# Kernel optimization log

Measured on AMD Instinct MI355X. Metric: run time of the kernel, lower is better.

The kernel has to match this reference:

```python
import jax, jax.numpy as jnp
import numpy as np

SEQ_LEN = 16384
D = 2048
K = 50          # tagset size
START = 48
STOP = 49
NEG = -10000.0


def setup_inputs() -> dict:
    key = jax.random.key(0)
    k1, k2, k3, k4 = jax.random.split(key, 4)
    input_var = jax.random.normal(k1, (SEQ_LEN, D), jnp.float32)
    tags = jax.random.randint(k2, (SEQ_LEN,), 0, 48, dtype=jnp.int32)  # real tags only
    W = jax.random.normal(k3, (K, D), jnp.float32) * 0.02              # hidden2tag weight
    b = jnp.zeros((K,), jnp.float32)                                   # hidden2tag bias
    transitions = jax.random.normal(k4, (K, K), jnp.float32) * 0.1
    # match the torch init: no transition into START, none out of STOP
    transitions = transitions.at[START, :].set(NEG).at[:, STOP].set(NEG)
    return {"input_var": input_var, "tags": tags, "W": W, "b": b, "transitions": transitions}


def reference(input_var, tags, W, b, transitions):
    # dropout in eval mode == identity (faithful deterministic forward)
    feats = input_var @ W.T + b  # [T, K] emission scores

    # --- CRF forward algorithm (log partition) ---
    alpha0 = jnp.full((K,), NEG, jnp.float32).at[START].set(0.0)

    def step(alpha, feat):
        # tag_var[i, j] = alpha[j] + transitions[i, j] + feat[i]
        s = alpha[None, :] + transitions           # [K, K]
        m = jnp.max(s, axis=1)                     # stable log-sum-exp
        alpha_new = feat + m + jnp.log(jnp.sum(jnp.exp(s - m[:, None]), axis=1))
        return alpha_new, None

    alpha, _ = jax.lax.scan(step, alpha0, feats)
    term = alpha + transitions[STOP]
    mt = jnp.max(term)
    forward_score = mt + jnp.log(jnp.sum(jnp.exp(term - mt)))

    # --- gold path score ---
    pad_start = jnp.concatenate([jnp.array([START], dtype=tags.dtype), tags])
    pad_stop = jnp.concatenate([tags, jnp.array([STOP], dtype=tags.dtype)])
    gold = (jnp.sum(transitions[pad_stop, pad_start])
            + jnp.sum(feats[jnp.arange(SEQ_LEN), tags]))

    return forward_score - gold
```

## Files before the change

kernel.cpp:

```cpp
#include <hip/hip_runtime.h>

typedef unsigned short u16;
typedef unsigned int u32;
typedef __bf16 b16x8 __attribute__((ext_vector_type(8)));
typedef float f32x16 __attribute__((ext_vector_type(16)));

#define SEQ   16384
#define DM    2048
#define KT    50
#define NST   48
#define NSP   49

__device__ __forceinline__ int perm64(int g){
  int q = (g>>2)&3;
  return (q==1 || q==2) ? (g^12) : g;
}
__device__ __forceinline__ u16 bfb(float f){
  __bf16 b = (__bf16)f;
  return __builtin_bit_cast(u16, b);
}
__device__ __forceinline__ int pk2(float a, float b){
  return (int)((u32)bfb(a) | ((u32)bfb(b) << 16));
}
__device__ __forceinline__ b16x8 cast8(int4 v){ return __builtin_bit_cast(b16x8, v); }

__device__ __forceinline__ f32x16 mfma_(b16x8 a, b16x8 b, f32x16 c){
  return __builtin_amdgcn_mfma_f32_32x32x16_bf16(a, b, c, 0, 0, 0);
}

__device__ __forceinline__ void mm64(const b16x8 A[2][4], const b16x8 B[4][2], f32x16 acc[2][2]){
#pragma unroll
  for (int mi=0; mi<2; ++mi)
#pragma unroll
    for (int ni=0; ni<2; ++ni){
      f32x16 a;
#pragma unroll
      for (int q=0;q<16;q++) a[q] = 0.0f;
#pragma unroll
      for (int kt=0; kt<4; ++kt) a = mfma_(A[mi][kt], B[kt][ni], a);
      acc[mi][ni] = a;
    }
}

__device__ __forceinline__ void repack(const f32x16 acc[2][2], b16x8 B[4][2]){
#pragma unroll
  for (int kb=0; kb<4; ++kb){
    const int mi = kb>>1, t = kb&1;
#pragma unroll
    for (int ni=0; ni<2; ++ni){
      int4 dw;
      dw.x = pk2(acc[mi][ni][8*t+0], acc[mi][ni][8*t+1]);
      dw.y = pk2(acc[mi][ni][8*t+2], acc[mi][ni][8*t+3]);
      dw.z = pk2(acc[mi][ni][8*t+4], acc[mi][ni][8*t+5]);
      dw.w = pk2(acc[mi][ni][8*t+6], acc[mi][ni][8*t+7]);
      B[kb][ni] = cast8(dw);
    }
  }
}

template<int PERM>
__device__ __forceinline__ void ident_frags(b16x8 B[4][2], int lane){
  const int h = lane>>5, j0 = lane&31;
#pragma unroll
  for (int kt=0; kt<4; ++kt)
#pragma unroll
    for (int ni=0; ni<2; ++ni){
      const int col = j0 + 32*ni;
      int d[4];
#pragma unroll
      for (int dd=0; dd<4; ++dd){
        int r0 = 16*kt + 8*h + 2*dd, r1 = r0 + 1;
        int p0 = PERM ? perm64(r0) : r0;
        int p1 = PERM ? perm64(r1) : r1;
        d[dd] = (int)((p0==col ? 0x3F80u : 0u) | ((p1==col ? 0x3F80u : 0u) << 16));
      }
      int4 v; v.x=d[0]; v.y=d[1]; v.z=d[2]; v.w=d[3];
      B[kt][ni] = cast8(v);
    }
}

__device__ __forceinline__ float acc_wave_max(const f32x16 acc[2][2]){
  float m = 0.0f;
#pragma unroll
  for (int mi=0;mi<2;mi++)
#pragma unroll
    for (int ni=0;ni<2;ni++)
#pragma unroll
      for (int q=0;q<16;q++) m = fmaxf(m, acc[mi][ni][q]);
#pragma unroll
  for (int o=32;o>=1;o>>=1) m = fmaxf(m, __shfl_xor(m, o, 64));
  return m;
}

template<int PROW>
__device__ __forceinline__ void store_mat_lds(u16* mat, const f32x16 acc[2][2], float inv, int lane){
  const int h = lane>>5, j0 = lane&31;
#pragma unroll
  for (int mi=0;mi<2;mi++)
#pragma unroll
    for (int ni=0;ni<2;ni++)
#pragma unroll
      for (int r=0;r<16;r++){
        int gp = 32*mi + (r&3) + 8*(r>>2) + 4*h;
        int a = PROW ? perm64(gp) : gp;
        int b = perm64(32*ni + j0);
        mat[a*64 + (b ^ ((a&7)<<3))] = bfb(acc[mi][ni][r]*inv);
      }
}
template<int PROW>
__device__ __forceinline__ void store_mat_glob(u16* mat, const f32x16 acc[2][2], float inv, int lane){
  const int h = lane>>5, j0 = lane&31;
#pragma unroll
  for (int mi=0;mi<2;mi++)
#pragma unroll
    for (int ni=0;ni<2;ni++)
#pragma unroll
      for (int r=0;r<16;r++){
        int gp = 32*mi + (r&3) + 8*(r>>2) + 4*h;
        int a = PROW ? perm64(gp) : gp;
        int b = perm64(32*ni + j0);
        mat[a*64 + b] = bfb(acc[mi][ni][r]*inv);
      }
}
__device__ __forceinline__ void load_afrag_lds(const u16* mat, b16x8 A[2][4], int lane){
  const int h = lane>>5, i0 = lane&31;
#pragma unroll
  for (int mi=0;mi<2;mi++)
#pragma unroll
    for (int kt=0;kt<4;kt++){
      int i = 32*mi + i0;
      int cb = (16*kt + 8*h) ^ ((i&7)<<3);
      A[mi][kt] = cast8(*(const int4*)(mat + i*64 + cb));
    }
}
__device__ __forceinline__ void load_afrag_glob(const u16* mat, b16x8 A[2][4], int lane){
  const int h = lane>>5, i0 = lane&31;
#pragma unroll
  for (int mi=0;mi<2;mi++)
#pragma unroll
    for (int kt=0;kt<4;kt++){
      int i = 32*mi + i0;
      A[mi][kt] = cast8(*(const int4*)(mat + i*64 + 16*kt + 8*h));
    }
}

__global__ void k_prep(const float* __restrict__ W, const float* __restrict__ T,
                       u16* __restrict__ Wp, u16* __restrict__ E){
  int tid = blockIdx.x*256 + threadIdx.x;
  int n = gridDim.x*256;
  for (int idx = tid; idx < 64*DM; idx += n){
    int r = idx >> 11, d = idx & 2047;
    Wp[idx] = (r < KT) ? bfb(W[r*DM + d]) : (u16)0;
  }
  for (int idx = tid; idx < 64*64; idx += n){
    int a = idx >> 6, b = idx & 63;
    int pa = perm64(a);
    E[idx] = (pa < KT && b < KT) ? bfb(__expf(T[pa*50 + b])) : (u16)0;
  }
}

__global__ __launch_bounds__(256, 2) void k_gemm(const float* __restrict__ in,
      const u16* __restrict__ Wp, const float* __restrict__ bias,
      const int* __restrict__ tags, float* __restrict__ feats, float* __restrict__ gout){
  const int w = threadIdx.x>>6, lane = threadIdx.x&63;
  const int h = lane>>5, i0 = lane&31;
  const int blk = blockIdx.x;
  const int row = blk*32 + i0;
  f32x16 acc0, acc1;
#pragma unroll
  for (int q=0;q<16;q++){ acc0[q]=0.f; acc1[q]=0.f; }
  const float* pa  = in + (size_t)row*DM + w*512 + 8*h;
  const u16*   pb0 = Wp + (size_t)i0*DM + w*512 + 8*h;
  const u16*   pb1 = Wp + (size_t)(i0+32)*DM + w*512 + 8*h;
#pragma unroll 4
  for (int s=0;s<32;s++){
    float4 fa = *(const float4*)(pa + s*16);
    float4 fb = *(const float4*)(pa + s*16 + 4);
    b16x8 av;
    av[0]=(__bf16)fa.x; av[1]=(__bf16)fa.y; av[2]=(__bf16)fa.z; av[3]=(__bf16)fa.w;
    av[4]=(__bf16)fb.x; av[5]=(__bf16)fb.y; av[6]=(__bf16)fb.z; av[7]=(__bf16)fb.w;
    b16x8 b0 = cast8(*(const int4*)(pb0 + s*16));
    b16x8 b1 = cast8(*(const int4*)(pb1 + s*16));
    acc0 = mfma_(av, b0, acc0);
    acc1 = mfma_(av, b1, acc1);
  }
  __shared__ float planes[4][32][64];
#pragma unroll
  for (int r=0;r<16;r++){
    int g = (r&3) + 8*(r>>2) + 4*h;
    planes[w][g][i0]    = acc0[r];
    planes[w][g][i0+32] = acc1[r];
  }
  __syncthreads();
  __shared__ float tile[32][66];
  for (int cidx = threadIdx.x; cidx < 2048; cidx += 256){
    int g = cidx>>6, c = cidx&63;
    float v = planes[0][g][c]+planes[1][g][c]+planes[2][g][c]+planes[3][g][c];
    tile[g][c] = (c<KT) ? (v + bias[c]) : -1e4f;
  }
  __syncthreads();
  __shared__ float mrow[32];
  if (threadIdx.x < 32){
    int g = threadIdx.x;
    float mx = -1e30f;
    for (int c=0;c<KT;c++) mx = fmaxf(mx, tile[g][c]);
    mrow[g] = mx;
    int t = blk*32 + g;
    gout[t] = tile[g][tags[t]] - mx;
  }
  __syncthreads();
  for (int cidx = threadIdx.x; cidx < 2048; cidx += 256){
    int g = cidx>>6, c = cidx&63;
    feats[(size_t)(blk*32+g)*64 + c] = (c<KT) ? (tile[g][c] - mrow[g]) : -1e4f;
  }
}

__global__ __launch_bounds__(512, 2) void k_scan(const float* __restrict__ feats,
        const u16* __restrict__ Emat, u16* __restrict__ M1, float* __restrict__ S1){
  const int w = threadIdx.x >> 6, lane = threadIdx.x & 63;
  const int h = lane>>5;
  const int blk = blockIdx.x;
  const int t0 = (blk*8 + w)*8;
  __shared__ __align__(16) float u_lds[8][64];
  __shared__ __align__(16) u16 mats[8][4096];
  __shared__ float logs[8];

  b16x8 Af[2][4];
  load_afrag_glob(Emat, Af, lane);
  b16x8 Bf[4][2];
  ident_frags<0>(Bf, lane);
  const int pl = perm64(lane);
  float x = feats[(size_t)t0*64 + pl];
  f32x16 acc[2][2];
#pragma unroll
  for (int s=0;s<8;s++){
    u_lds[w][lane] = __expf(x);
    if (s<7) x = feats[(size_t)(t0+s+1)*64 + pl];
    mm64(Af, Bf, acc);
    float uu0[16], uu1[16];
#pragma unroll
    for (int k2=0;k2<4;k2++){
      float4 v0 = *(const float4*)&u_lds[w][      8*k2 + 4*h];
      float4 v1 = *(const float4*)&u_lds[w][32 +  8*k2 + 4*h];
      uu0[4*k2+0]=v0.x; uu0[4*k2+1]=v0.y; uu0[4*k2+2]=v0.z; uu0[4*k2+3]=v0.w;
      uu1[4*k2+0]=v1.x; uu1[4*k2+1]=v1.y; uu1[4*k2+2]=v1.z; uu1[4*k2+3]=v1.w;
    }
#pragma unroll
    for (int ni=0;ni<2;ni++)
#pragma unroll
      for (int r=0;r<16;r++){
        acc[0][ni][r] *= uu0[r];
        acc[1][ni][r] *= uu1[r];
      }
    repack(acc, Bf);
  }
  float m = acc_wave_max(acc);
  float inv = 1.0f/m;
  store_mat_lds<1>(mats[w], acc, inv, lane);
  if (lane==0) logs[w] = __logf(m);
  __syncthreads();
  if (w==0){
    float slog = logs[0]+logs[1]+logs[2]+logs[3]+logs[4]+logs[5]+logs[6]+logs[7];
    b16x8 Bc[4][2]; ident_frags<1>(Bc, lane);
    f32x16 a2[2][2];
#pragma unroll 1
    for (int m8=0;m8<8;m8++){
      b16x8 Am[2][4];
      load_afrag_lds(mats[m8], Am, lane);
      mm64(Am, Bc, a2);
      repack(a2, Bc);
    }
    float m2 = acc_wave_max(a2);
    slog += __logf(m2);
    store_mat_glob<0>(M1 + (size_t)blk*4096, a2, 1.0f/m2, lane);
    if (lane==0) S1[blk] = slog;
  }
}

__global__ __launch_bounds__(64) void k_comb8(const u16* __restrict__ Min, const float* __restrict__ Sin,
      u16* __restrict__ Mout, float* __restrict__ Sout){
  const int lane = threadIdx.x & 63;
  const int blk = blockIdx.x;
  b16x8 Bc[4][2]; ident_frags<1>(Bc, lane);
  f32x16 a2[2][2];
  float slog = 0.f;
#pragma unroll 1
  for (int m=0;m<8;m++){
    b16x8 Am[2][4];
    load_afrag_glob(Min + (size_t)(blk*8+m)*4096, Am, lane);
    slog += Sin[blk*8+m];
    mm64(Am, Bc, a2);
    repack(a2, Bc);
  }
  float mx = acc_wave_max(a2);
  slog += __logf(mx);
  store_mat_glob<0>(Mout + (size_t)blk*4096, a2, 1.0f/mx, lane);
  if (lane==0) Sout[blk] = slog;
}

__global__ __launch_bounds__(512, 2) void k_final(const u16* __restrict__ M2, const float* __restrict__ S2,
      const float* __restrict__ T, const int* __restrict__ tags,
      const float* __restrict__ gvec, float* __restrict__ out){
  const int w = threadIdx.x>>6, lane = threadIdx.x&63;
  __shared__ __align__(16) u16 mats[8][4096];
  __shared__ float logs[8];
  __shared__ float alpha[64];
  __shared__ float red[512];
  __shared__ float slog_sh;
  {
    b16x8 Bc[4][2]; ident_frags<1>(Bc, lane);
    f32x16 a2[2][2];
    float sl = 0.f;
#pragma unroll 1
    for (int m=0;m<4;m++){
      b16x8 Am[2][4];
      load_afrag_glob(M2 + (size_t)(w*4+m)*4096, Am, lane);
      sl += S2[w*4+m];
      mm64(Am, Bc, a2);
      repack(a2, Bc);
    }
    float mx = acc_wave_max(a2);
    sl += __logf(mx);
    store_mat_lds<0>(mats[w], a2, 1.0f/mx, lane);
    if (lane==0) logs[w] = sl;
  }
  __syncthreads();
  if (w==0){
    b16x8 Bc[4][2]; ident_frags<1>(Bc, lane);
    f32x16 a2[2][2];
#pragma unroll 1
    for (int m=0;m<8;m++){
      b16x8 Am[2][4];
      load_afrag_lds(mats[m], Am, lane);
      mm64(Am, Bc, a2);
      repack(a2, Bc);
    }
    float sl = logs[0]+logs[1]+logs[2]+logs[3]+logs[4]+logs[5]+logs[6]+logs[7];
    if ((lane&31)==16){
      const int h = lane>>5;
#pragma unroll
      for (int mi=0;mi<2;mi++)
#pragma unroll
        for (int r=0;r<16;r++){
          int gp = 32*mi + (r&3) + 8*(r>>2) + 4*h;
          alpha[gp] = a2[mi][1][r];
        }
    }
    if (lane==0) slog_sh = sl;
  }
  float part = 0.f;
  for (int t = threadIdx.x; t < SEQ; t += 512) part += gvec[t];
  for (int idx = threadIdx.x; idx < SEQ+1; idx += 512){
    int s0 = (idx==0) ? NST : tags[idx-1];
    int s1 = (idx<SEQ) ? tags[idx] : NSP;
    part += T[s1*50 + s0];
  }
  red[threadIdx.x] = part;
  for (int st=256; st>0; st>>=1){
    __syncthreads();
    if (threadIdx.x < st) red[threadIdx.x] += red[threadIdx.x + st];
  }
  __syncthreads();
  if (threadIdx.x < 64){
    float a = alpha[lane];
    float term = (lane < KT && a > 0.f) ? (__logf(a) + slog_sh + T[NSP*50 + lane]) : -1e30f;
    float tm = term;
#pragma unroll
    for (int o=32;o>=1;o>>=1) tm = fmaxf(tm, __shfl_xor(tm, o, 64));
    float e = __expf(term - tm);
#pragma unroll
    for (int o=32;o>=1;o>>=1) e += __shfl_xor(e, o, 64);
    if (threadIdx.x == 0) out[0] = (tm + __logf(e)) - red[0];
  }
}

extern "C" void kernel_launch(void* const* d_in, const int* in_sizes, int n_in,
                              void* d_out, int out_size, void* d_ws, size_t ws_size,
                              hipStream_t stream) {
  (void)in_sizes; (void)n_in; (void)out_size; (void)ws_size;
  const float* input = (const float*)d_in[0];
  const int*   tags  = (const int*)  d_in[1];
  const float* W     = (const float*)d_in[2];
  const float* bias  = (const float*)d_in[3];
  const float* T     = (const float*)d_in[4];

  char* ws = (char*)d_ws;
  float* feats = (float*)(ws + 0);
  float* gvec  = (float*)(ws + 4194304);
  u16*   Wp    = (u16*)  (ws + 4259840);
  u16*   Emat  = (u16*)  (ws + 4521984);
  u16*   M1    = (u16*)  (ws + 4530176);
  float* S1    = (float*)(ws + 6627328);
  u16*   M2    = (u16*)  (ws + 6628352);
  float* S2    = (float*)(ws + 6890496);

  k_prep <<<256, 256, 0, stream>>>(W, T, Wp, Emat);
  k_gemm <<<512, 256, 0, stream>>>(input, Wp, bias, tags, feats, gvec);
  k_scan <<<256, 512, 0, stream>>>(feats, Emat, M1, S1);
  k_comb8<<<32,  64,  0, stream>>>(M1, S1, M2, S2);
  k_final<<<1,   512, 0, stream>>>(M2, S2, T, tags, gvec, (float*)d_out);
}
```

Measured before the change: 111.0 us.

## Fuse CRF pipeline into two kernels with LDS-tiled GEMM and last-block reduction

Collapses five launches into two. The prep kernel is removed: W is converted to bf16 inside a new double-buffered, LDS-swizzled GEMM with 64-row tiles, and exp(T) is built in LDS per scan block. The gold-path score is folded into the GEMM as per-block partials. The scan does 16 steps per wave with half the blocks, and the comb8 and final stages run inside the last-arriving scan block via an atomic counter. This cuts launch overhead and intermediate global traffic, but it serialises the final reduction on one block and relies on an atomic counter that is reset by GEMM block 0.

```diff
diff --git a/kernel.cpp b/kernel.cpp
--- a/kernel.cpp
+++ b/kernel.cpp
@@ -53,6 +53,21 @@
       dw.y = pk2(acc[mi][ni][8*t+2], acc[mi][ni][8*t+3]);
       dw.z = pk2(acc[mi][ni][8*t+4], acc[mi][ni][8*t+5]);
       dw.w = pk2(acc[mi][ni][8*t+6], acc[mi][ni][8*t+7]);
+      B[kb][ni] = cast8(dw);
+    }
+  }
+}
+__device__ __forceinline__ void repack_s(const f32x16 acc[2][2], b16x8 B[4][2], float s){
+#pragma unroll
+  for (int kb=0; kb<4; ++kb){
+    const int mi = kb>>1, t = kb&1;
+#pragma unroll
+    for (int ni=0; ni<2; ++ni){
+      int4 dw;
+      dw.x = pk2(acc[mi][ni][8*t+0]*s, acc[mi][ni][8*t+1]*s);
+      dw.y = pk2(acc[mi][ni][8*t+2]*s, acc[mi][ni][8*t+3]*s);
+      dw.z = pk2(acc[mi][ni][8*t+4]*s, acc[mi][ni][8*t+5]*s);
+      dw.w = pk2(acc[mi][ni][8*t+6]*s, acc[mi][ni][8*t+7]*s);
       B[kb][ni] = cast8(dw);
     }
   }
@@ -144,98 +159,147 @@
     }
 }
 
-__global__ void k_prep(const float* __restrict__ W, const float* __restrict__ T,
-                       u16* __restrict__ Wp, u16* __restrict__ E){
-  int tid = blockIdx.x*256 + threadIdx.x;
-  int n = gridDim.x*256;
-  for (int idx = tid; idx < 64*DM; idx += n){
-    int r = idx >> 11, d = idx & 2047;
-    Wp[idx] = (r < KT) ? bfb(W[r*DM + d]) : (u16)0;
-  }
-  for (int idx = tid; idx < 64*64; idx += n){
-    int a = idx >> 6, b = idx & 63;
-    int pa = perm64(a);
-    E[idx] = (pa < KT && b < KT) ? bfb(__expf(T[pa*50 + b])) : (u16)0;
-  }
-}
-
-__global__ __launch_bounds__(256, 2) void k_gemm(const float* __restrict__ in,
-      const u16* __restrict__ Wp, const float* __restrict__ bias,
-      const int* __restrict__ tags, float* __restrict__ feats, float* __restrict__ gout){
-  const int w = threadIdx.x>>6, lane = threadIdx.x&63;
-  const int h = lane>>5, i0 = lane&31;
-  const int blk = blockIdx.x;
-  const int row = blk*32 + i0;
-  f32x16 acc0, acc1;
-#pragma unroll
-  for (int q=0;q<16;q++){ acc0[q]=0.f; acc1[q]=0.f; }
-  const float* pa  = in + (size_t)row*DM + w*512 + 8*h;
-  const u16*   pb0 = Wp + (size_t)i0*DM + w*512 + 8*h;
-  const u16*   pb1 = Wp + (size_t)(i0+32)*DM + w*512 + 8*h;
-#pragma unroll 4
-  for (int s=0;s<32;s++){
-    float4 fa = *(const float4*)(pa + s*16);
-    float4 fb = *(const float4*)(pa + s*16 + 4);
-    b16x8 av;
-    av[0]=(__bf16)fa.x; av[1]=(__bf16)fa.y; av[2]=(__bf16)fa.z; av[3]=(__bf16)fa.w;
-    av[4]=(__bf16)fb.x; av[5]=(__bf16)fb.y; av[6]=(__bf16)fb.z; av[7]=(__bf16)fb.w;
-    b16x8 b0 = cast8(*(const int4*)(pb0 + s*16));
-    b16x8 b1 = cast8(*(const int4*)(pb1 + s*16));
-    acc0 = mfma_(av, b0, acc0);
-    acc1 = mfma_(av, b1, acc1);
-  }
-  __shared__ float planes[4][32][64];
+__global__ __launch_bounds__(512, 2) void k_gemm(const float* __restrict__ in,
+      const int* __restrict__ tags, const float* __restrict__ W,
+      const float* __restrict__ bias, const float* __restrict__ T,
+      float* __restrict__ feats, float* __restrict__ gpart, int* __restrict__ counter){
+  __shared__ __align__(16) char smem[65536];
+  u16* const bA = (u16*)smem;
+  u16* const bB = (u16*)(smem + 32768);
+  const int t = threadIdx.x;
+  const int w = t>>6, lane = t&63;
+  const int j0 = lane&31, h = lane>>5;
+  const int rh = w&1, ch = (w>>1)&1, kq = (w>>2)&1;
+  const int row0 = blockIdx.x*64;
+  const int aswz = (j0&7)<<3;
+  if (blockIdx.x==0 && t==0) *counter = 0;
+
+  float rA[2][8], rB[2][8];
+  f32x16 acc;
+#pragma unroll
+  for (int q=0;q<16;q++) acc[q]=0.f;
+
+#define LOADCHUNK(kc)                                                       \
+  { _Pragma("unroll")                                                       \
+    for (int i=0;i<2;i++){                                                  \
+      int g=(i<<9)+t; int r=g>>4, c8=g&15;                                  \
+      const float* p = in + (size_t)(row0+r)*DM + (kc)*128 + c8*8;          \
+      float4 f0=*(const float4*)p, f1=*(const float4*)(p+4);                \
+      rA[i][0]=f0.x; rA[i][1]=f0.y; rA[i][2]=f0.z; rA[i][3]=f0.w;           \
+      rA[i][4]=f1.x; rA[i][5]=f1.y; rA[i][6]=f1.z; rA[i][7]=f1.w;           \
+      if (r < KT){                                                          \
+        const float* q2 = W + (size_t)r*DM + (kc)*128 + c8*8;               \
+        float4 g0=*(const float4*)q2, g1=*(const float4*)(q2+4);            \
+        rB[i][0]=g0.x; rB[i][1]=g0.y; rB[i][2]=g0.z; rB[i][3]=g0.w;         \
+        rB[i][4]=g1.x; rB[i][5]=g1.y; rB[i][6]=g1.z; rB[i][7]=g1.w;         \
+      } else {                                                              \
+        _Pragma("unroll") for (int z=0;z<8;z++) rB[i][z]=0.f;               \
+      }                                                                     \
+    } }
+#define WRITECHUNK(d)                                                       \
+  { _Pragma("unroll")                                                       \
+    for (int i=0;i<2;i++){                                                  \
+      int g=(i<<9)+t; int r=g>>4, c8=g&15;                                  \
+      int off = r*128 + ((c8*8) ^ ((r&7)<<3));                              \
+      int4 da; da.x=pk2(rA[i][0],rA[i][1]); da.y=pk2(rA[i][2],rA[i][3]);    \
+      da.z=pk2(rA[i][4],rA[i][5]); da.w=pk2(rA[i][6],rA[i][7]);             \
+      *(int4*)(bA + (d)*8192 + off) = da;                                   \
+      int4 db; db.x=pk2(rB[i][0],rB[i][1]); db.y=pk2(rB[i][2],rB[i][3]);    \
+      db.z=pk2(rB[i][4],rB[i][5]); db.w=pk2(rB[i][6],rB[i][7]);             \
+      *(int4*)(bB + (d)*8192 + off) = db;                                   \
+    } }
+
+  LOADCHUNK(0); WRITECHUNK(0);
+  __syncthreads();
+  for (int kc=0; kc<16; ++kc){
+    const int d = kc & 1;
+    if (kc < 15) LOADCHUNK(kc+1);
+    const u16* Arow = bA + d*8192 + (32*rh + j0)*128;
+    const u16* Brow = bB + d*8192 + (32*ch + j0)*128;
+#pragma unroll
+    for (int kk=0;kk<4;kk++){
+      const int kt = kq*4 + kk;
+      b16x8 aF = cast8(*(const int4*)(Arow + ((kt*16 + h*8) ^ aswz)));
+      b16x8 bF = cast8(*(const int4*)(Brow + ((kt*16 + h*8) ^ aswz)));
+      acc = mfma_(aF, bF, acc);
+    }
+    if (kc < 15) WRITECHUNK(d^1);
+    __syncthreads();
+  }
+#undef LOADCHUNK
+#undef WRITECHUNK
+
+  float* planes = (float*)smem;
+  float* tile   = (float*)(smem + 32768);
+  float* mrow   = (float*)(smem + 49664);
 #pragma unroll
   for (int r=0;r<16;r++){
-    int g = (r&3) + 8*(r>>2) + 4*h;
-    planes[w][g][i0]    = acc0[r];
-    planes[w][g][i0+32] = acc1[r];
-  }
-  __syncthreads();
-  __shared__ float tile[32][66];
-  for (int cidx = threadIdx.x; cidx < 2048; cidx += 256){
+    int gp = (r&3) + 8*(r>>2) + 4*h;
+    planes[kq*4096 + (32*rh + gp)*64 + 32*ch + j0] = acc[r];
+  }
+  __syncthreads();
+  for (int cidx = t; cidx < 4096; cidx += 512){
     int g = cidx>>6, c = cidx&63;
-    float v = planes[0][g][c]+planes[1][g][c]+planes[2][g][c]+planes[3][g][c];
-    tile[g][c] = (c<KT) ? (v + bias[c]) : -1e4f;
-  }
-  __syncthreads();
-  __shared__ float mrow[32];
-  if (threadIdx.x < 32){
-    int g = threadIdx.x;
+    float v = planes[cidx] + planes[4096 + cidx];
+    tile[g*66+c] = (c<KT) ? (v + bias[c]) : -1e4f;
+  }
+  __syncthreads();
+  if (t < 64){
+    int g = t;
     float mx = -1e30f;
-    for (int c=0;c<KT;c++) mx = fmaxf(mx, tile[g][c]);
+    for (int c=0;c<KT;c++) mx = fmaxf(mx, tile[g*66+c]);
     mrow[g] = mx;
-    int t = blk*32 + g;
-    gout[t] = tile[g][tags[t]] - mx;
-  }
-  __syncthreads();
-  for (int cidx = threadIdx.x; cidx < 2048; cidx += 256){
+    int tt = row0 + g;
+    int s1 = tags[tt];
+    int s0 = (tt==0) ? NST : tags[tt-1];
+    float part = (tile[g*66 + s1] - mx) + T[s1*50 + s0];
+    if (tt == SEQ-1) part += T[NSP*50 + s1];
+#pragma unroll
+    for (int o=32;o>=1;o>>=1) part += __shfl_xor(part, o, 64);
+    if (t==0) gpart[blockIdx.x] = part;
+  }
+  __syncthreads();
+  for (int cidx = t; cidx < 4096; cidx += 512){
     int g = cidx>>6, c = cidx&63;
-    feats[(size_t)(blk*32+g)*64 + c] = (c<KT) ? (tile[g][c] - mrow[g]) : -1e4f;
+    feats[(size_t)(row0+g)*64 + c] = (c<KT) ? (tile[g*66+c] - mrow[g]) : -1e4f;
   }
 }
 
 __global__ __launch_bounds__(512, 2) void k_scan(const float* __restrict__ feats,
-        const u16* __restrict__ Emat, u16* __restrict__ M1, float* __restrict__ S1){
-  const int w = threadIdx.x >> 6, lane = threadIdx.x & 63;
+        const float* __restrict__ T, const float* __restrict__ gpart,
+        int* __restrict__ counter, u16* __restrict__ M1, float* __restrict__ S1,
+        float* __restrict__ out){
+  const int t = threadIdx.x;
+  const int w = t>>6, lane = t&63;
   const int h = lane>>5;
   const int blk = blockIdx.x;
-  const int t0 = (blk*8 + w)*8;
+  __shared__ __align__(16) u16 E_lds[4096];
   __shared__ __align__(16) float u_lds[8][64];
   __shared__ __align__(16) u16 mats[8][4096];
   __shared__ float logs[8];
+  __shared__ float alpha[64];
+  __shared__ int bcast;
+
+  for (int idx = t; idx < 4096; idx += 512){
+    int a = idx>>6, b = idx&63;
+    int pa = perm64(a);
+    float v = (pa<KT && b<KT) ? __expf(T[pa*50 + b]) : 0.f;
+    E_lds[a*64 + (b ^ ((a&7)<<3))] = bfb(v);
+  }
+  __syncthreads();
 
   b16x8 Af[2][4];
-  load_afrag_glob(Emat, Af, lane);
+  load_afrag_lds(E_lds, Af, lane);
   b16x8 Bf[4][2];
   ident_frags<0>(Bf, lane);
   const int pl = perm64(lane);
+  const int t0 = (blk*8 + w)*16;
   float x = feats[(size_t)t0*64 + pl];
   f32x16 acc[2][2];
 #pragma unroll
-  for (int s=0;s<8;s++){
+  for (int s=0;s<16;s++){
     u_lds[w][lane] = __expf(x);
-    if (s<7) x = feats[(size_t)(t0+s+1)*64 + pl];
+    if (s<15) x = feats[(size_t)(t0+s+1)*64 + pl];
     mm64(Af, Bf, acc);
     float uu0[16], uu1[16];
 #pragma unroll
@@ -255,8 +319,7 @@
     repack(acc, Bf);
   }
   float m = acc_wave_max(acc);
-  float inv = 1.0f/m;
-  store_mat_lds<1>(mats[w], acc, inv, lane);
+  store_mat_lds<1>(mats[w], acc, 1.0f/m, lane);
   if (lane==0) logs[w] = __logf(m);
   __syncthreads();
   if (w==0){
@@ -275,49 +338,37 @@
     store_mat_glob<0>(M1 + (size_t)blk*4096, a2, 1.0f/m2, lane);
     if (lane==0) S1[blk] = slog;
   }
-}
-
-__global__ __launch_bounds__(64) void k_comb8(const u16* __restrict__ Min, const float* __restrict__ Sin,
-      u16* __restrict__ Mout, float* __restrict__ Sout){
-  const int lane = threadIdx.x & 63;
-  const int blk = blockIdx.x;
-  b16x8 Bc[4][2]; ident_frags<1>(Bc, lane);
-  f32x16 a2[2][2];
-  float slog = 0.f;
-#pragma unroll 1
-  for (int m=0;m<8;m++){
-    b16x8 Am[2][4];
-    load_afrag_glob(Min + (size_t)(blk*8+m)*4096, Am, lane);
-    slog += Sin[blk*8+m];
-    mm64(Am, Bc, a2);
-    repack(a2, Bc);
-  }
-  float mx = acc_wave_max(a2);
-  slog += __logf(mx);
-  store_mat_glob<0>(Mout + (size_t)blk*4096, a2, 1.0f/mx, lane);
-  if (lane==0) Sout[blk] = slog;
-}
-
-__global__ __launch_bounds__(512, 2) void k_final(const u16* __restrict__ M2, const float* __restrict__ S2,
-      const float* __restrict__ T, const int* __restrict__ tags,
-      const float* __restrict__ gvec, float* __restrict__ out){
-  const int w = threadIdx.x>>6, lane = threadIdx.x&63;
-  __shared__ __align__(16) u16 mats[8][4096];
-  __shared__ float logs[8];
-  __shared__ float alpha[64];
-  __shared__ float red[512];
-  __shared__ float slog_sh;
+  __syncthreads();
+  if (t==0){
+    __threadfence();
+    bcast = atomicAdd(counter, 1);
+  }
+  __syncthreads();
+  if (bcast != gridDim.x - 1) return;
+  __threadfence();
+
   {
     b16x8 Bc[4][2]; ident_frags<1>(Bc, lane);
     f32x16 a2[2][2];
     float sl = 0.f;
+    b16x8 Acur[2][4], Anx[2][4];
+    load_afrag_glob(M1 + (size_t)(w*16)*4096, Acur, lane);
 #pragma unroll 1
-    for (int m=0;m<4;m++){
-      b16x8 Am[2][4];
-      load_afrag_glob(M2 + (size_t)(w*4+m)*4096, Am, lane);
-      sl += S2[w*4+m];
-      mm64(Am, Bc, a2);
-      repack(a2, Bc);
+    for (int mm=0; mm<16; mm++){
+      if (mm<15) load_afrag_glob(M1 + (size_t)(w*16+mm+1)*4096, Anx, lane);
+      sl += S1[w*16+mm];
+      mm64(Acur, Bc, a2);
+      if (mm==7){
+        float mx = acc_wave_max(a2);
+        sl += __logf(mx);
+        repack_s(a2, Bc, 1.0f/mx);
+      } else {
+        repack(a2, Bc);
+      }
+#pragma unroll
+      for (int mi=0;mi<2;mi++)
+#pragma unroll
+        for (int kt=0;kt<4;kt++) Acur[mi][kt] = Anx[mi][kt];
     }
     float mx = acc_wave_max(a2);
     sl += __logf(mx);
@@ -329,15 +380,14 @@
     b16x8 Bc[4][2]; ident_frags<1>(Bc, lane);
     f32x16 a2[2][2];
 #pragma unroll 1
-    for (int m=0;m<8;m++){
+    for (int m8=0;m8<8;m8++){
       b16x8 Am[2][4];
-      load_afrag_lds(mats[m], Am, lane);
+      load_afrag_lds(mats[m8], Am, lane);
       mm64(Am, Bc, a2);
       repack(a2, Bc);
     }
-    float sl = logs[0]+logs[1]+logs[2]+logs[3]+logs[4]+logs[5]+logs[6]+logs[7];
+    float slog = logs[0]+logs[1]+logs[2]+logs[3]+logs[4]+logs[5]+logs[6]+logs[7];
     if ((lane&31)==16){
-      const int h = lane>>5;
 #pragma unroll
       for (int mi=0;mi<2;mi++)
 #pragma unroll
@@ -346,31 +396,18 @@
           alpha[gp] = a2[mi][1][r];
         }
     }
-    if (lane==0) slog_sh = sl;
-  }
-  float part = 0.f;
-  for (int t = threadIdx.x; t < SEQ; t += 512) part += gvec[t];
-  for (int idx = threadIdx.x; idx < SEQ+1; idx += 512){
-    int s0 = (idx==0) ? NST : tags[idx-1];
-    int s1 = (idx<SEQ) ? tags[idx] : NSP;
-    part += T[s1*50 + s0];
-  }
-  red[threadIdx.x] = part;
-  for (int st=256; st>0; st>>=1){
-    __syncthreads();
-    if (threadIdx.x < st) red[threadIdx.x] += red[threadIdx.x + st];
-  }
-  __syncthreads();
-  if (threadIdx.x < 64){
+    float gold = gpart[lane] + gpart[lane+64] + gpart[lane+128] + gpart[lane+192];
+#pragma unroll
+    for (int o=32;o>=1;o>>=1) gold += __shfl_xor(gold, o, 64);
     float a = alpha[lane];
-    float term = (lane < KT && a > 0.f) ? (__logf(a) + slog_sh + T[NSP*50 + lane]) : -1e30f;
+    float term = (lane < KT && a > 0.f) ? (__logf(a) + slog + T[NSP*50 + lane]) : -1e30f;
     float tm = term;
 #pragma unroll
     for (int o=32;o>=1;o>>=1) tm = fmaxf(tm, __shfl_xor(tm, o, 64));
     float e = __expf(term - tm);
 #pragma unroll
     for (int o=32;o>=1;o>>=1) e += __shfl_xor(e, o, 64);
-    if (threadIdx.x == 0) out[0] = (tm + __logf(e)) - red[0];
+    if (lane==0) out[0] = (tm + __logf(e)) - gold;
   }
 }
 
@@ -385,18 +422,12 @@
   const float* T     = (const float*)d_in[4];
 
   char* ws = (char*)d_ws;
-  float* feats = (float*)(ws + 0);
-  float* gvec  = (float*)(ws + 4194304);
-  u16*   Wp    = (u16*)  (ws + 4259840);
-  u16*   Emat  = (u16*)  (ws + 4521984);
-  u16*   M1    = (u16*)  (ws + 4530176);
-  float* S1    = (float*)(ws + 6627328);
-  u16*   M2    = (u16*)  (ws + 6628352);
-  float* S2    = (float*)(ws + 6890496);
-
-  k_prep <<<256, 256, 0, stream>>>(W, T, Wp, Emat);
-  k_gemm <<<512, 256, 0, stream>>>(input, Wp, bias, tags, feats, gvec);
-  k_scan <<<256, 512, 0, stream>>>(feats, Emat, M1, S1);
-  k_comb8<<<32,  64,  0, stream>>>(M1, S1, M2, S2);
-  k_final<<<1,   512, 0, stream>>>(M2, S2, T, tags, gvec, (float*)d_out);
-}
+  float* feats   = (float*)(ws + 0);
+  float* gpart   = (float*)(ws + 4194304);
+  int*   counter = (int*)  (ws + 4195328);
+  u16*   M1      = (u16*)  (ws + 4195840);
+  float* S1      = (float*)(ws + 5244416);
+
+  k_gemm<<<256, 512, 0, stream>>>(input, tags, W, bias, T, feats, gpart, counter);
+  k_scan<<<128, 512, 0, stream>>>(feats, T, gpart, counter, M1, S1, (float*)d_out);
+}
```

New measurement: 97.59 us (median of 2 runs). 1.14x faster.
